# Kernel tuning notes

Hardware: AMD Instinct MI355X
Metric: run time of the kernel (lower is better)

## Reference

```python
import jax, jax.numpy as jnp
import numpy as np

B, C, H, W = 16, 64, 128, 128
C8 = C // 8

def setup_inputs() -> dict:
    key = jax.random.key(0)
    ks = jax.random.split(key, 9)
    s = 0.05
    return {
        "x": jax.random.normal(ks[0], (B, C, H, W), jnp.float32),
        "y": jax.random.normal(ks[1], (B, C, H, W), jnp.float32),
        "query_w": jax.random.normal(ks[2], (C8, C), jnp.float32) * s,
        "query_b": jax.random.normal(ks[3], (C8,), jnp.float32) * s,
        "key_w": jax.random.normal(ks[4], (C8, C), jnp.float32) * s,
        "key_b": jax.random.normal(ks[5], (C8,), jnp.float32) * s,
        "value_w": jax.random.normal(ks[6], (C, 2 * C), jnp.float32) * s,
        "value_b": jax.random.normal(ks[7], (C,), jnp.float32) * s,
        "gamma": jax.random.normal(ks[8], (), jnp.float32) * 0.1,
    }

def _conv1x1(t, w, b):
    # t: [B, Cin, H, W], w: [Cout, Cin] -> [B, Cout, H, W]
    return jnp.einsum('oc,bchw->bohw', w, t) + b[None, :, None, None]

def reference(x, y, query_w, query_b, key_w, key_b, value_w, value_b, gamma):
    b, c, h, w = x.shape
    q = _conv1x1(x, query_w, query_b)                       # [B, C8, H, W]
    k = _conv1x1(y, key_w, key_b)                           # [B, C8, H, W]
    v = _conv1x1(jnp.concatenate([x, y], axis=1), value_w, value_b)  # [B, C, H, W]

    # axial energies: H-axis (g indexes key rows), W-axis (u indexes key cols)
    energy_H = jnp.einsum('bchw,bcgw->bhwg', q, k)          # [B, H, W, H]
    energy_W = jnp.einsum('bchw,bchu->bhwu', q, k)          # [B, H, W, W]

    # -inf on the H diagonal (self position counted once, via the W branch)
    eye = jnp.eye(h, dtype=bool)                            # [H, H]
    energy_H = jnp.where(eye[None, :, None, :], -jnp.inf, energy_H)

    att = jax.nn.softmax(jnp.concatenate([energy_H, energy_W], axis=3), axis=3)
    att_H = att[..., :h]                                    # [B, H, W, H]
    att_W = att[..., h:]                                    # [B, H, W, W]

    out_H = jnp.einsum('bcgw,bhwg->bchw', v, att_H)
    out_W = jnp.einsum('bchu,bhwu->bchw', v, att_W)
    return gamma * (out_H + out_W) + x + y
```

## Files before the change

### kernel.cpp

```cpp
#include <hip/hip_runtime.h>

#define NCH 80
#define HW 16384

typedef unsigned short u16;
typedef unsigned int u32;
typedef short s16x8 __attribute__((ext_vector_type(8)));
typedef float f32x4 __attribute__((ext_vector_type(4)));

__device__ __forceinline__ float b2f_lo(u32 pk){ union{u32 u; float f;} c; c.u = pk<<16; return c.f; }
__device__ __forceinline__ float b2f_hi(u32 pk){ union{u32 u; float f;} c; c.u = pk & 0xffff0000u; return c.f; }
__device__ __forceinline__ float b2f(u16 v){ union{u32 u; float f;} c; c.u = ((u32)v)<<16; return c.f; }
__device__ __forceinline__ u16 f2b_hw(float f){
    union{ __bf16 h; u16 s; } c; c.h = (__bf16)f; return c.s;
}
__device__ __forceinline__ u32 pk2(float a, float b){
    return (u32)f2b_hw(a) | ((u32)f2b_hw(b)<<16);
}
#define NEG_INF (-__builtin_inff())

union U4S8 { uint4 u; s16x8 v; };

__global__ __launch_bounds__(256) void k_wcvt(
    const float* __restrict__ qw, const float* __restrict__ qb,
    const float* __restrict__ kw, const float* __restrict__ kb,
    const float* __restrict__ vw, const float* __restrict__ vb,
    u16* __restrict__ wbf, float* __restrict__ bias80)
{
    int i = blockIdx.x*256 + threadIdx.x;
    int ch = i >> 7, cin = i & 127;
    float v;
    if (ch < 8)       v = (cin < 64) ? qw[ch*64 + cin] : 0.f;
    else if (ch < 16) v = (cin >= 64) ? kw[(ch-8)*64 + (cin-64)] : 0.f;
    else              v = vw[(ch-16)*128 + cin];
    wbf[i] = f2b_hw(v);
    if (i < 80){
        bias80[i] = (i<8) ? qb[i] : (i<16) ? kb[i-8] : vb[i-16];
    }
}

__global__ __launch_bounds__(256, 4) void k_qkv_mfma(
    const float* __restrict__ x, const float* __restrict__ y,
    const u16* __restrict__ wbf, const float* __restrict__ bias80,
    u16* __restrict__ qkv, u16* __restrict__ xy)
{
    __shared__ u32 a32[128*65];

    int t = threadIdx.x;
    int p0 = blockIdx.x * 128;
    int b = p0 >> 14, rem = p0 & 16383;
    const float* xb = x + (size_t)b*64*HW + rem;
    const float* yb = y + (size_t)b*64*HW + rem;

    #pragma unroll
    for (int r=0;r<8;r++){
        int idx = t + r*256;
        int cp = idx >> 5;
        int pxg = (idx & 31) * 4;
        const float* srcp = (cp < 32) ? xb : yb;
        int c0 = (cp & 31)*2;
        float4 fa = *(const float4*)&srcp[(size_t)c0*HW + pxg];
        float4 fb = *(const float4*)&srcp[(size_t)(c0+1)*HW + pxg];
        a32[(pxg+0)*65 + cp] = pk2(fa.x, fb.x);
        a32[(pxg+1)*65 + cp] = pk2(fa.y, fb.y);
        a32[(pxg+2)*65 + cp] = pk2(fa.z, fb.z);
        a32[(pxg+3)*65 + cp] = pk2(fa.w, fb.w);
    }
    __syncthreads();

    if (xy){
        #pragma unroll
        for (int r=0;r<16;r++){
            int idx = t + r*256;
            int c = idx >> 6;
            int pxp = idx & 63;
            int cpx = c >> 1, cpy = 32 + (c >> 1);
            u32 wx0 = a32[(2*pxp)*65 + cpx], wx1 = a32[(2*pxp+1)*65 + cpx];
            u32 wy0 = a32[(2*pxp)*65 + cpy], wy1 = a32[(2*pxp+1)*65 + cpy];
            float xv0 = (c&1)? b2f_hi(wx0) : b2f_lo(wx0);
            float xv1 = (c&1)? b2f_hi(wx1) : b2f_lo(wx1);
            float yv0 = (c&1)? b2f_hi(wy0) : b2f_lo(wy0);
            float yv1 = (c&1)? b2f_hi(wy1) : b2f_lo(wy1);
            size_t xw = ((size_t)(b*64+c)*HW + rem) >> 1;
            ((u32*)xy)[xw + pxp] = pk2(xv0+yv0, xv1+yv1);
        }
    }

    int wv = t >> 6, l = t & 63;
    int lm = l & 15, lq = l >> 4;

    #pragma unroll
    for (int m2=0;m2<2;m2++){
        int pxl = (wv*2 + m2)*16 + lm;
        s16x8 af[4];
        #pragma unroll
        for (int ks=0;ks<4;ks++){
            int wbase = pxl*65 + ks*16 + lq*4;
            U4S8 uu;
            uu.u = make_uint4(a32[wbase], a32[wbase+1], a32[wbase+2], a32[wbase+3]);
            af[ks] = uu.v;
        }
        #pragma unroll
        for (int nt=0;nt<5;nt++){
            int ch = nt*16 + lm;
            const u16* wrow = wbf + ch*128 + lq*8;
            f32x4 acc = (f32x4){0.f,0.f,0.f,0.f};
            #pragma unroll
            for (int ks=0;ks<4;ks++){
                s16x8 bfrag = *(const s16x8*)(wrow + ks*32);
                acc = __builtin_amdgcn_mfma_f32_16x16x32_bf16(af[ks], bfrag, acc, 0, 0, 0);
            }
            float bs = bias80[ch];
            int pxs = (wv*2+m2)*16 + lq*4;
            u32 lo = pk2(acc[0]+bs, acc[1]+bs);
            u32 hi = pk2(acc[2]+bs, acc[3]+bs);
            *(uint2*)&qkv[(size_t)(b*NCH + ch)*HW + rem + pxs] = make_uint2(lo, hi);
        }
    }
}

__global__ __launch_bounds__(256) void k_tr(const u16* __restrict__ src, u16* __restrict__ dst)
{
    __shared__ u16 tile[64][65];
    int blk = blockIdx.x;
    int plane = blk >> 2, tq = blk & 3;
    int r0 = (tq >> 1) * 64, c0 = (tq & 1) * 64;
    const u16* s = src + (size_t)plane * HW;
    u16* d = dst + (size_t)plane * HW;
    int col = threadIdx.x & 63, rr = threadIdx.x >> 6;
    #pragma unroll
    for (int k=0;k<16;k++){
        int r = k*4 + rr;
        tile[r][col] = s[(r0+r)*128 + c0 + col];
    }
    __syncthreads();
    #pragma unroll
    for (int k=0;k<16;k++){
        int r = k*4 + rr;
        d[(c0+r)*128 + r0 + col] = tile[col][r];
    }
}

__global__ __launch_bounds__(512, 4) void k_col(
    const u16* __restrict__ qkvT, u16* __restrict__ colT,
    float* __restrict__ mH, float* __restrict__ sH)
{
    __shared__ __align__(16) float q_s[8*128];
    __shared__ __align__(16) float k_sw[8*128];
    __shared__ __align__(16) u16  v_bf[64*128];
    __shared__ __align__(16) u16  p_bf[128*128];

    int t = threadIdx.x;
    int b = blockIdx.x >> 7, w = blockIdx.x & 127;
    const u32* src = (const u32*)(qkvT + (size_t)b*NCH*HW + w*128);
    u32* v32 = (u32*)v_bf;
    u32* p32 = (u32*)p_bf;

    #pragma unroll
    for (int r=0;r<2;r++){
        int idx = t + r*512;
        int ch = idx >> 6, hp = idx & 63;
        u32 pk = src[ch*8192 + hp];
        int g0 = hp*2;
        if (ch < 8){
            *(float2*)&q_s[ch*128 + g0] = make_float2(b2f_lo(pk), b2f_hi(pk));
        } else {
            int o = ch - 8;
            k_sw[g0*8     + (o ^ ((g0>>3)&7))]     = b2f_lo(pk);
            k_sw[(g0+1)*8 + (o ^ (((g0+1)>>3)&7))] = b2f_hi(pk);
        }
    }
    #pragma unroll
    for (int r=0;r<8;r++){
        int idx = t + r*512;
        int c = idx >> 6, gp = idx & 63;
        v32[(c*64 + gp) ^ ((c&7)<<2)] = src[(16+c)*8192 + gp];
    }
    __syncthreads();

    int tr = t >> 4, tc = t & 15;
    int h0 = tr*4, g0 = tc*8;
    float e[4][8];
    #pragma unroll
    for (int i=0;i<4;i++)
        #pragma unroll
        for (int j=0;j<8;j++) e[i][j] = 0.f;

    #pragma unroll
    for (int o=0;o<8;o++){
        float qv[4], kv[8];
        #pragma unroll
        for (int i=0;i<4;i++) qv[i] = q_s[o*128 + h0 + i];
        int kb = o ^ (tc & 7);
        #pragma unroll
        for (int j=0;j<8;j++) kv[j] = k_sw[(g0+j)*8 + kb];
        #pragma unroll
        for (int i=0;i<4;i++)
            #pragma unroll
            for (int j=0;j<8;j++) e[i][j] += qv[i]*kv[j];
    }
    #pragma unroll
    for (int i=0;i<4;i++){
        int h = h0 + i;
        if ((h>>3) == tc) e[i][h&7] = NEG_INF;
    }
    #pragma unroll
    for (int i=0;i<4;i++){
        int h = h0 + i;
        float m = e[i][0];
        #pragma unroll
        for (int j=1;j<8;j++) m = fmaxf(m, e[i][j]);
        m = fmaxf(m, __shfl_xor(m,1));
        m = fmaxf(m, __shfl_xor(m,2));
        m = fmaxf(m, __shfl_xor(m,4));
        m = fmaxf(m, __shfl_xor(m,8));
        float s = 0.f;
        #pragma unroll
        for (int j=0;j<8;j++){ float pp = __expf(e[i][j]-m); e[i][j]=pp; s += pp; }
        s += __shfl_xor(s,1);
        s += __shfl_xor(s,2);
        s += __shfl_xor(s,4);
        s += __shfl_xor(s,8);
        if (tc == 0){
            mH[b*HW + h*128 + w] = m;
            sH[b*HW + h*128 + w] = s;
        }
        uint4 pw;
        pw.x = pk2(e[i][0], e[i][1]);
        pw.y = pk2(e[i][2], e[i][3]);
        pw.z = pk2(e[i][4], e[i][5]);
        pw.w = pk2(e[i][6], e[i][7]);
        *(uint4*)&p32[(h*64 + tc*4) ^ ((h&7)<<2)] = pw;
    }
    __syncthreads();

    int wv = t >> 6, l = t & 63;
    int lm = l & 15, lq = l >> 4;
    int mt = wv;
    f32x4 acc[4];
    #pragma unroll
    for (int nt=0; nt<4; nt++) acc[nt] = (f32x4){0.f,0.f,0.f,0.f};

    #pragma unroll
    for (int ks=0; ks<4; ks++){
        int ri = mt*16 + lm;
        s16x8 a = *(const s16x8*)&p32[(ri*64 + ks*16 + lq*4) ^ ((ri&7)<<2)];
        #pragma unroll
        for (int nt=0; nt<4; nt++){
            int c = nt*16 + lm;
            s16x8 bf_ = *(const s16x8*)&v32[(c*64 + ks*16 + lq*4) ^ ((c&7)<<2)];
            acc[nt] = __builtin_amdgcn_mfma_f32_16x16x32_bf16(a, bf_, acc[nt], 0, 0, 0);
        }
    }
    #pragma unroll
    for (int nt=0; nt<4; nt++){
        int c = nt*16 + lm;
        int hh = mt*16 + lq*4;
        uint2 st;
        st.x = pk2(acc[nt][0], acc[nt][1]);
        st.y = pk2(acc[nt][2], acc[nt][3]);
        *(uint2*)&colT[((size_t)(b*64+c)*128 + w)*128 + hh] = st;
    }
}

__global__ __launch_bounds__(512, 4) void k_row(
    const u16* __restrict__ qkv, const u16* __restrict__ colpart,
    const float* __restrict__ mH, const float* __restrict__ sH,
    const float* __restrict__ x, const float* __restrict__ y,
    const u16* __restrict__ xy,
    const float* __restrict__ gamma_p, float* __restrict__ out)
{
    __shared__ __align__(16) float q_s[8*128];
    __shared__ __align__(16) float k_sw[8*128];
    __shared__ __align__(16) u16  v_bf[64*128];
    __shared__ __align__(16) u16  p_bf[128*128];
    __shared__ float fc_s[128], fr_s[128];

    int t = threadIdx.x;
    int b = blockIdx.x >> 7, h = blockIdx.x & 127;
    const u32* src = (const u32*)(qkv + (size_t)b*NCH*HW + h*128);
    u32* v32 = (u32*)v_bf;
    u32* p32 = (u32*)p_bf;

    #pragma unroll
    for (int r=0;r<2;r++){
        int idx = t + r*512;
        int ch = idx >> 6, wp = idx & 63;
        u32 pk = src[ch*8192 + wp];
        int u0 = wp*2;
        if (ch < 8){
            *(float2*)&q_s[ch*128 + u0] = make_float2(b2f_lo(pk), b2f_hi(pk));
        } else {
            int o = ch - 8;
            k_sw[u0*8     + (o ^ ((u0>>3)&7))]     = b2f_lo(pk);
            k_sw[(u0+1)*8 + (o ^ (((u0+1)>>3)&7))] = b2f_hi(pk);
        }
    }
    #pragma unroll
    for (int r=0;r<8;r++){
        int idx = t + r*512;
        int c = idx >> 6, up = idx & 63;
        v32[(c*64 + up) ^ ((c&7)<<2)] = src[(16+c)*8192 + up];
    }
    __syncthreads();

    int tr = t >> 4, tc = t & 15;
    int w0 = tr*4, u0 = tc*8;
    float e[4][8];
    #pragma unroll
    for (int i=0;i<4;i++)
        #pragma unroll
        for (int j=0;j<8;j++) e[i][j] = 0.f;

    #pragma unroll
    for (int o=0;o<8;o++){
        float qv[4], kv[8];
        #pragma unroll
        for (int i=0;i<4;i++) qv[i] = q_s[o*128 + w0 + i];
        int kb = o ^ (tc & 7);
        #pragma unroll
        for (int j=0;j<8;j++) kv[j] = k_sw[(u0+j)*8 + kb];
        #pragma unroll
        for (int i=0;i<4;i++)
            #pragma unroll
            for (int j=0;j<8;j++) e[i][j] += qv[i]*kv[j];
    }
    int pixbase = b*HW + h*128;
    #pragma unroll
    for (int i=0;i<4;i++){
        int wp = w0 + i;
        float m = e[i][0];
        #pragma unroll
        for (int j=1;j<8;j++) m = fmaxf(m, e[i][j]);
        m = fmaxf(m, __shfl_xor(m,1));
        m = fmaxf(m, __shfl_xor(m,2));
        m = fmaxf(m, __shfl_xor(m,4));
        m = fmaxf(m, __shfl_xor(m,8));
        float mh = mH[pixbase + wp];
        float sh = sH[pixbase + wp];
        float mg = fmaxf(m, mh);
        float s = 0.f;
        #pragma unroll
        for (int j=0;j<8;j++){ float pp = __expf(e[i][j]-mg); e[i][j]=pp; s += pp; }
        s += __shfl_xor(s,1);
        s += __shfl_xor(s,2);
        s += __shfl_xor(s,4);
        s += __shfl_xor(s,8);
        if (tc == 0){
            float ef = __expf(mh - mg);
            float stot = sh*ef + s;
            fc_s[wp] = ef/stot;
            fr_s[wp] = 1.0f/stot;
        }
        uint4 pw;
        pw.x = pk2(e[i][0], e[i][1]);
        pw.y = pk2(e[i][2], e[i][3]);
        pw.z = pk2(e[i][4], e[i][5]);
        pw.w = pk2(e[i][6], e[i][7]);
        *(uint4*)&p32[(wp*64 + tc*4) ^ ((wp&7)<<2)] = pw;
    }
    __syncthreads();

    int wv = t >> 6, l = t & 63;
    int lm = l & 15, lq = l >> 4;
    int mt = wv;
    f32x4 acc[4];
    #pragma unroll
    for (int nt=0; nt<4; nt++) acc[nt] = (f32x4){0.f,0.f,0.f,0.f};

    #pragma unroll
    for (int ks=0; ks<4; ks++){
        int ri = mt*16 + lm;
        s16x8 a = *(const s16x8*)&p32[(ri*64 + ks*16 + lq*4) ^ ((ri&7)<<2)];
        #pragma unroll
        for (int nt=0; nt<4; nt++){
            int c = nt*16 + lm;
            s16x8 bf_ = *(const s16x8*)&v32[(c*64 + ks*16 + lq*4) ^ ((c&7)<<2)];
            acc[nt] = __builtin_amdgcn_mfma_f32_16x16x32_bf16(a, bf_, acc[nt], 0, 0, 0);
        }
    }
    float gm = gamma_p[0];
    int wq0 = mt*16 + lq*4;
    float fcv[4], frv[4];
    #pragma unroll
    for (int r2=0;r2<4;r2++){ fcv[r2] = fc_s[wq0+r2]; frv[r2] = fr_s[wq0+r2]; }

    #pragma unroll
    for (int nt=0; nt<4; nt++){
        int c = nt*16 + lm;
        size_t off = ((size_t)(b*64+c)*128 + h)*128 + wq0;
        uint2 cpv = *(const uint2*)&colpart[off];
        float cp[4] = {b2f_lo(cpv.x), b2f_hi(cpv.x), b2f_lo(cpv.y), b2f_hi(cpv.y)};
        float xs[4];
        if (xy){
            uint2 xv = *(const uint2*)&xy[off];
            xs[0]=b2f_lo(xv.x); xs[1]=b2f_hi(xv.x); xs[2]=b2f_lo(xv.y); xs[3]=b2f_hi(xv.y);
        } else {
            float4 x4 = *(const float4*)&x[off];
            float4 y4 = *(const float4*)&y[off];
            xs[0]=x4.x+y4.x; xs[1]=x4.y+y4.y; xs[2]=x4.z+y4.z; xs[3]=x4.w+y4.w;
        }
        float4 o4;
        o4.x = gm*(cp[0]*fcv[0] + acc[nt][0]*frv[0]) + xs[0];
        o4.y = gm*(cp[1]*fcv[1] + acc[nt][1]*frv[1]) + xs[1];
        o4.z = gm*(cp[2]*fcv[2] + acc[nt][2]*frv[2]) + xs[2];
        o4.w = gm*(cp[3]*fcv[3] + acc[nt][3]*frv[3]) + xs[3];
        *(float4*)&out[off] = o4;
    }
}

extern "C" void kernel_launch(void* const* d_in, const int* in_sizes, int n_in,
                              void* d_out, int out_size, void* d_ws, size_t ws_size,
                              hipStream_t stream)
{
    (void)in_sizes; (void)n_in; (void)out_size;
    const float* x  = (const float*)d_in[0];
    const float* y  = (const float*)d_in[1];
    const float* qw = (const float*)d_in[2];
    const float* qb = (const float*)d_in[3];
    const float* kw = (const float*)d_in[4];
    const float* kb = (const float*)d_in[5];
    const float* vw = (const float*)d_in[6];
    const float* vb = (const float*)d_in[7];
    const float* gm = (const float*)d_in[8];
    float* out = (float*)d_out;

    char* ws = (char*)d_ws;
    u16* qkv     = (u16*)(ws);
    u16* qkvT    = (u16*)(ws + 41943040ull);
    u16* colT    = (u16*)(ws + 83886080ull);
    u16* colpart = qkvT;
    float* mH    = (float*)(ws + 117440512ull);
    float* sH    = (float*)(ws + 118489088ull);
    u16* wbf     = (u16*)(ws + 119537664ull);
    float* bias80= (float*)(ws + 119558144ull);
    u16* xybuf   = nullptr;
    if (ws_size >= 119603200ull + 33554432ull)
        xybuf = (u16*)(ws + 119603200ull);

    k_wcvt<<<40, 256, 0, stream>>>(qw, qb, kw, kb, vw, vb, wbf, bias80);
    k_qkv_mfma<<<2048, 256, 0, stream>>>(x, y, wbf, bias80, qkv, xybuf);
    k_tr <<<5120, 256, 0, stream>>>(qkv, qkvT);
    k_col<<<2048, 512, 0, stream>>>(qkvT, colT, mH, sH);
    k_tr <<<4096, 256, 0, stream>>>(colT, colpart);
    k_row<<<2048, 512, 0, stream>>>(qkv, colpart, mH, sH, x, y, xybuf, gm, out);
}
```

Measured before the change: 180.7 us.

## Restructure QKV projection kernel LDS layout and fuse x+y sum into load phase

Changes the shared-memory staging buffer from pixel-major to channel-pair-major with a 132-word stride, so global loads store to LDS as 128-bit vectors. The x+y bf16 sum is now computed from registers during the load phase, which removes a second LDS read pass. Weight fragments are loaded once per channel tile and reused across two pixel tiles, with two interleaved accumulators. The occupancy hint is dropped from launch bounds, and register pressure rises from holding all loads in flight.

```diff
diff --git a/kernel.cpp b/kernel.cpp
--- a/kernel.cpp
+++ b/kernel.cpp
@@ -39,12 +39,12 @@
     }
 }
 
-__global__ __launch_bounds__(256, 4) void k_qkv_mfma(
+__global__ __launch_bounds__(256) void k_qkv_mfma(
     const float* __restrict__ x, const float* __restrict__ y,
     const u16* __restrict__ wbf, const float* __restrict__ bias80,
     u16* __restrict__ qkv, u16* __restrict__ xy)
 {
-    __shared__ u32 a32[128*65];
+    __shared__ u32 a32[64*132];
 
     int t = threadIdx.x;
     int p0 = blockIdx.x * 128;
@@ -52,70 +52,91 @@
     const float* xb = x + (size_t)b*64*HW + rem;
     const float* yb = y + (size_t)b*64*HW + rem;
 
-    #pragma unroll
-    for (int r=0;r<8;r++){
+    float4 fx0[4], fx1[4], fy0[4], fy1[4];
+    #pragma unroll
+    for (int r=0;r<4;r++){
         int idx = t + r*256;
         int cp = idx >> 5;
         int pxg = (idx & 31) * 4;
-        const float* srcp = (cp < 32) ? xb : yb;
-        int c0 = (cp & 31)*2;
-        float4 fa = *(const float4*)&srcp[(size_t)c0*HW + pxg];
-        float4 fb = *(const float4*)&srcp[(size_t)(c0+1)*HW + pxg];
-        a32[(pxg+0)*65 + cp] = pk2(fa.x, fb.x);
-        a32[(pxg+1)*65 + cp] = pk2(fa.y, fb.y);
-        a32[(pxg+2)*65 + cp] = pk2(fa.z, fb.z);
-        a32[(pxg+3)*65 + cp] = pk2(fa.w, fb.w);
-    }
-    __syncthreads();
-
-    if (xy){
-        #pragma unroll
-        for (int r=0;r<16;r++){
-            int idx = t + r*256;
-            int c = idx >> 6;
-            int pxp = idx & 63;
-            int cpx = c >> 1, cpy = 32 + (c >> 1);
-            u32 wx0 = a32[(2*pxp)*65 + cpx], wx1 = a32[(2*pxp+1)*65 + cpx];
-            u32 wy0 = a32[(2*pxp)*65 + cpy], wy1 = a32[(2*pxp+1)*65 + cpy];
-            float xv0 = (c&1)? b2f_hi(wx0) : b2f_lo(wx0);
-            float xv1 = (c&1)? b2f_hi(wx1) : b2f_lo(wx1);
-            float yv0 = (c&1)? b2f_hi(wy0) : b2f_lo(wy0);
-            float yv1 = (c&1)? b2f_hi(wy1) : b2f_lo(wy1);
-            size_t xw = ((size_t)(b*64+c)*HW + rem) >> 1;
-            ((u32*)xy)[xw + pxp] = pk2(xv0+yv0, xv1+yv1);
-        }
-    }
+        const float* xp = xb + (size_t)(2*cp)*HW + pxg;
+        const float* yp = yb + (size_t)(2*cp)*HW + pxg;
+        fx0[r] = *(const float4*)xp;
+        fx1[r] = *(const float4*)(xp + HW);
+        fy0[r] = *(const float4*)yp;
+        fy1[r] = *(const float4*)(yp + HW);
+    }
+    #pragma unroll
+    for (int r=0;r<4;r++){
+        int idx = t + r*256;
+        int cp = idx >> 5;
+        int pxg = (idx & 31) * 4;
+        uint4 wx, wy;
+        wx.x = pk2(fx0[r].x, fx1[r].x);
+        wx.y = pk2(fx0[r].y, fx1[r].y);
+        wx.z = pk2(fx0[r].z, fx1[r].z);
+        wx.w = pk2(fx0[r].w, fx1[r].w);
+        wy.x = pk2(fy0[r].x, fy1[r].x);
+        wy.y = pk2(fy0[r].y, fy1[r].y);
+        wy.z = pk2(fy0[r].z, fy1[r].z);
+        wy.w = pk2(fy0[r].w, fy1[r].w);
+        *(uint4*)&a32[cp*132 + pxg]       = wx;
+        *(uint4*)&a32[(32+cp)*132 + pxg]  = wy;
+        if (xy){
+            uint2 s0, s1;
+            s0.x = pk2(fx0[r].x+fy0[r].x, fx0[r].y+fy0[r].y);
+            s0.y = pk2(fx0[r].z+fy0[r].z, fx0[r].w+fy0[r].w);
+            s1.x = pk2(fx1[r].x+fy1[r].x, fx1[r].y+fy1[r].y);
+            s1.y = pk2(fx1[r].z+fy1[r].z, fx1[r].w+fy1[r].w);
+            *(uint2*)&xy[(size_t)(b*64 + 2*cp)*HW + rem + pxg]     = s0;
+            *(uint2*)&xy[(size_t)(b*64 + 2*cp+1)*HW + rem + pxg]   = s1;
+        }
+    }
+    __syncthreads();
 
     int wv = t >> 6, l = t & 63;
     int lm = l & 15, lq = l >> 4;
 
+    s16x8 af[2][4];
     #pragma unroll
     for (int m2=0;m2<2;m2++){
         int pxl = (wv*2 + m2)*16 + lm;
-        s16x8 af[4];
         #pragma unroll
         for (int ks=0;ks<4;ks++){
-            int wbase = pxl*65 + ks*16 + lq*4;
+            int cpb = (ks&1)*16 + lq*4 + ((ks>>1)*32);
             U4S8 uu;
-            uu.u = make_uint4(a32[wbase], a32[wbase+1], a32[wbase+2], a32[wbase+3]);
-            af[ks] = uu.v;
-        }
-        #pragma unroll
-        for (int nt=0;nt<5;nt++){
-            int ch = nt*16 + lm;
-            const u16* wrow = wbf + ch*128 + lq*8;
-            f32x4 acc = (f32x4){0.f,0.f,0.f,0.f};
-            #pragma unroll
-            for (int ks=0;ks<4;ks++){
-                s16x8 bfrag = *(const s16x8*)(wrow + ks*32);
-                acc = __builtin_amdgcn_mfma_f32_16x16x32_bf16(af[ks], bfrag, acc, 0, 0, 0);
-            }
-            float bs = bias80[ch];
-            int pxs = (wv*2+m2)*16 + lq*4;
-            u32 lo = pk2(acc[0]+bs, acc[1]+bs);
-            u32 hi = pk2(acc[2]+bs, acc[3]+bs);
-            *(uint2*)&qkv[(size_t)(b*NCH + ch)*HW + rem + pxs] = make_uint2(lo, hi);
-        }
+            uu.u = make_uint4(a32[(cpb+0)*132 + pxl], a32[(cpb+1)*132 + pxl],
+                              a32[(cpb+2)*132 + pxl], a32[(cpb+3)*132 + pxl]);
+            af[m2][ks] = uu.v;
+        }
+    }
+
+    #pragma unroll
+    for (int nt=0;nt<5;nt++){
+        int ch = nt*16 + lm;
+        const u16* wrow = wbf + ch*128 + lq*8;
+        s16x8 b0 = *(const s16x8*)(wrow);
+        s16x8 b1 = *(const s16x8*)(wrow + 32);
+        s16x8 b2 = *(const s16x8*)(wrow + 64);
+        s16x8 b3 = *(const s16x8*)(wrow + 96);
+        f32x4 acc0 = (f32x4){0.f,0.f,0.f,0.f};
+        f32x4 acc1 = (f32x4){0.f,0.f,0.f,0.f};
+        acc0 = __builtin_amdgcn_mfma_f32_16x16x32_bf16(af[0][0], b0, acc0, 0,0,0);
+        acc1 = __builtin_amdgcn_mfma_f32_16x16x32_bf16(af[1][0], b0, acc1, 0,0,0);
+        acc0 = __builtin_amdgcn_mfma_f32_16x16x32_bf16(af[0][1], b1, acc0, 0,0,0);
+        acc1 = __builtin_amdgcn_mfma_f32_16x16x32_bf16(af[1][1], b1, acc1, 0,0,0);
+        acc0 = __builtin_amdgcn_mfma_f32_16x16x32_bf16(af[0][2], b2, acc0, 0,0,0);
+        acc1 = __builtin_amdgcn_mfma_f32_16x16x32_bf16(af[1][2], b2, acc1, 0,0,0);
+        acc0 = __builtin_amdgcn_mfma_f32_16x16x32_bf16(af[0][3], b3, acc0, 0,0,0);
+        acc1 = __builtin_amdgcn_mfma_f32_16x16x32_bf16(af[1][3], b3, acc1, 0,0,0);
+        float bs = bias80[ch];
+        size_t chbase = (size_t)(b*NCH + ch)*HW + rem;
+        uint2 st0, st1;
+        st0.x = pk2(acc0[0]+bs, acc0[1]+bs);
+        st0.y = pk2(acc0[2]+bs, acc0[3]+bs);
+        st1.x = pk2(acc1[0]+bs, acc1[1]+bs);
+        st1.y = pk2(acc1[2]+bs, acc1[3]+bs);
+        *(uint2*)&qkv[chbase + (wv*2+0)*16 + lq*4] = st0;
+        *(uint2*)&qkv[chbase + (wv*2+1)*16 + lq*4] = st1;
     }
 }
 
```

Measured after the change: 165.5 us. 8.4% less time.

## Load QKV projection inputs directly into LDS with swizzled fp32 layout

Applied to the files above, without the earlier changes.

The QKV projection kernel now uses global_load_lds to move fp32 x/y tiles straight into shared memory in an XOR-swizzled layout. It no longer packs them to bf16 through registers on the way in. The bf16 conversion moves to the MFMA fragment read, and the tile per block shrinks from 128 to 64 pixels, so the grid doubles. This is meant to cut register and VALU work in the load phase and raise occupancy, at the cost of more scalar LDS reads per fragment and more blocks each reloading the weights.

```diff
diff --git a/kernel.cpp b/kernel.cpp
--- a/kernel.cpp
+++ b/kernel.cpp
@@ -10,7 +10,6 @@
 
 __device__ __forceinline__ float b2f_lo(u32 pk){ union{u32 u; float f;} c; c.u = pk<<16; return c.f; }
 __device__ __forceinline__ float b2f_hi(u32 pk){ union{u32 u; float f;} c; c.u = pk & 0xffff0000u; return c.f; }
-__device__ __forceinline__ float b2f(u16 v){ union{u32 u; float f;} c; c.u = ((u32)v)<<16; return c.f; }
 __device__ __forceinline__ u16 f2b_hw(float f){
     union{ __bf16 h; u16 s; } c; c.h = (__bf16)f; return c.s;
 }
@@ -20,6 +19,18 @@
 #define NEG_INF (-__builtin_inff())
 
 union U4S8 { uint4 u; s16x8 v; };
+
+__device__ __forceinline__ int swz_px(int cin, int px){
+    int q = cin >> 3;
+    return px ^ ((q & 3) << 2) ^ ((q & 1) << 4);
+}
+
+__device__ __forceinline__ void gload_lds16(const void* g, void* l){
+    __builtin_amdgcn_global_load_lds(
+        (const __attribute__((address_space(1))) void*)g,
+        (__attribute__((address_space(3))) void*)l,
+        16, 0, 0);
+}
 
 __global__ __launch_bounds__(256) void k_wcvt(
     const float* __restrict__ qw, const float* __restrict__ qb,
@@ -39,82 +50,79 @@
     }
 }
 
-__global__ __launch_bounds__(256, 4) void k_qkv_mfma(
+__global__ __launch_bounds__(256) void k_qkv_mfma(
     const float* __restrict__ x, const float* __restrict__ y,
     const u16* __restrict__ wbf, const float* __restrict__ bias80,
     u16* __restrict__ qkv, u16* __restrict__ xy)
 {
-    __shared__ u32 a32[128*65];
+    __shared__ float xs_lds[128*64];
 
     int t = threadIdx.x;
-    int p0 = blockIdx.x * 128;
+    int wv = t >> 6, l = t & 63;
+    int p0 = blockIdx.x * 64;
     int b = p0 >> 14, rem = p0 & 16383;
+
     const float* xb = x + (size_t)b*64*HW + rem;
     const float* yb = y + (size_t)b*64*HW + rem;
 
     #pragma unroll
-    for (int r=0;r<8;r++){
-        int idx = t + r*256;
-        int cp = idx >> 5;
-        int pxg = (idx & 31) * 4;
-        const float* srcp = (cp < 32) ? xb : yb;
-        int c0 = (cp & 31)*2;
-        float4 fa = *(const float4*)&srcp[(size_t)c0*HW + pxg];
-        float4 fb = *(const float4*)&srcp[(size_t)(c0+1)*HW + pxg];
-        a32[(pxg+0)*65 + cp] = pk2(fa.x, fb.x);
-        a32[(pxg+1)*65 + cp] = pk2(fa.y, fb.y);
-        a32[(pxg+2)*65 + cp] = pk2(fa.z, fb.z);
-        a32[(pxg+3)*65 + cp] = pk2(fa.w, fb.w);
-    }
-    __syncthreads();
+    for (int i=0;i<8;i++){
+        int s = wv*8 + i;
+        int cin = s*4 + (l>>4);
+        int pxg = swz_px(cin, (l&15)*4);
+        const float* gp = (cin < 64) ? (xb + (size_t)cin*HW + pxg)
+                                     : (yb + (size_t)(cin-64)*HW + pxg);
+        gload_lds16(gp, (char*)xs_lds + s*1024);
+    }
+    __syncthreads();
+
+    int lm = l & 15, lq = l >> 4;
+    int px = wv*16 + lm;
+
+    s16x8 af[4];
+    #pragma unroll
+    for (int ks=0; ks<4; ks++){
+        float fv[8];
+        #pragma unroll
+        for (int j=0;j<8;j++){
+            int cin = ks*32 + lq*8 + j;
+            fv[j] = xs_lds[cin*64 + swz_px(cin, px)];
+        }
+        U4S8 uu;
+        uu.u = make_uint4(pk2(fv[0],fv[1]), pk2(fv[2],fv[3]),
+                          pk2(fv[4],fv[5]), pk2(fv[6],fv[7]));
+        af[ks] = uu.v;
+    }
+
+    #pragma unroll
+    for (int nt=0;nt<5;nt++){
+        int ch = nt*16 + lm;
+        const u16* wrow = wbf + ch*128 + lq*8;
+        f32x4 acc = (f32x4){0.f,0.f,0.f,0.f};
+        #pragma unroll
+        for (int ks=0;ks<4;ks++){
+            s16x8 bfrag = *(const s16x8*)(wrow + ks*32);
+            acc = __builtin_amdgcn_mfma_f32_16x16x32_bf16(af[ks], bfrag, acc, 0,0,0);
+        }
+        float bs = bias80[ch];
+        uint2 st;
+        st.x = pk2(acc[0]+bs, acc[1]+bs);
+        st.y = pk2(acc[2]+bs, acc[3]+bs);
+        *(uint2*)&qkv[(size_t)(b*NCH + ch)*HW + rem + wv*16 + lq*4] = st;
+    }
 
     if (xy){
-        #pragma unroll
-        for (int r=0;r<16;r++){
-            int idx = t + r*256;
-            int c = idx >> 6;
-            int pxp = idx & 63;
-            int cpx = c >> 1, cpy = 32 + (c >> 1);
-            u32 wx0 = a32[(2*pxp)*65 + cpx], wx1 = a32[(2*pxp+1)*65 + cpx];
-            u32 wy0 = a32[(2*pxp)*65 + cpy], wy1 = a32[(2*pxp+1)*65 + cpy];
-            float xv0 = (c&1)? b2f_hi(wx0) : b2f_lo(wx0);
-            float xv1 = (c&1)? b2f_hi(wx1) : b2f_lo(wx1);
-            float yv0 = (c&1)? b2f_hi(wy0) : b2f_lo(wy0);
-            float yv1 = (c&1)? b2f_hi(wy1) : b2f_lo(wy1);
-            size_t xw = ((size_t)(b*64+c)*HW + rem) >> 1;
-            ((u32*)xy)[xw + pxp] = pk2(xv0+yv0, xv1+yv1);
-        }
-    }
-
-    int wv = t >> 6, l = t & 63;
-    int lm = l & 15, lq = l >> 4;
-
-    #pragma unroll
-    for (int m2=0;m2<2;m2++){
-        int pxl = (wv*2 + m2)*16 + lm;
-        s16x8 af[4];
-        #pragma unroll
-        for (int ks=0;ks<4;ks++){
-            int wbase = pxl*65 + ks*16 + lq*4;
-            U4S8 uu;
-            uu.u = make_uint4(a32[wbase], a32[wbase+1], a32[wbase+2], a32[wbase+3]);
-            af[ks] = uu.v;
-        }
-        #pragma unroll
-        for (int nt=0;nt<5;nt++){
-            int ch = nt*16 + lm;
-            const u16* wrow = wbf + ch*128 + lq*8;
-            f32x4 acc = (f32x4){0.f,0.f,0.f,0.f};
-            #pragma unroll
-            for (int ks=0;ks<4;ks++){
-                s16x8 bfrag = *(const s16x8*)(wrow + ks*32);
-                acc = __builtin_amdgcn_mfma_f32_16x16x32_bf16(af[ks], bfrag, acc, 0, 0, 0);
-            }
-            float bs = bias80[ch];
-            int pxs = (wv*2+m2)*16 + lq*4;
-            u32 lo = pk2(acc[0]+bs, acc[1]+bs);
-            u32 hi = pk2(acc[2]+bs, acc[3]+bs);
-            *(uint2*)&qkv[(size_t)(b*NCH + ch)*HW + rem + pxs] = make_uint2(lo, hi);
+        u32* xyp = (u32*)xy;
+        #pragma unroll
+        for (int r=0;r<8;r++){
+            int oi = t + r*256;
+            int ch = oi >> 5;
+            int pxp = oi & 31;
+            int wx = ch*64 + swz_px(ch, 2*pxp);
+            int wyi = (ch+64)*64 + swz_px(ch+64, 2*pxp);
+            float2 xv = *(float2*)&xs_lds[wx];
+            float2 yv = *(float2*)&xs_lds[wyi];
+            xyp[((size_t)(b*64+ch)*HW + rem)/2 + pxp] = pk2(xv.x+yv.x, xv.y+yv.y);
         }
     }
 }
@@ -439,7 +447,7 @@
         xybuf = (u16*)(ws + 119603200ull);
 
     k_wcvt<<<40, 256, 0, stream>>>(qw, qb, kw, kb, vw, vb, wbf, bias80);
-    k_qkv_mfma<<<2048, 256, 0, stream>>>(x, y, wbf, bias80, qkv, xybuf);
+    k_qkv_mfma<<<4096, 256, 0, stream>>>(x, y, wbf, bias80, qkv, xybuf);
     k_tr <<<5120, 256, 0, stream>>>(qkv, qkvT);
     k_col<<<2048, 512, 0, stream>>>(qkvT, colT, mH, sH);
     k_tr <<<4096, 256, 0, stream>>>(colT, colpart);
```

Result: slower. 187.5 us (+3.7%).
